# Kernel optimization log

Measured on AMD Instinct MI355X. Metric: run time of the kernel, lower is better.

## Reference

```python
import jax, jax.numpy as jnp
import numpy as np

# batches, users-per-batch (max_user_num), servers-per-batch (max_server_num), dims
B, U, S, DU, DS, H = 64, 256, 64, 16, 16, 256
DEG_S, DEG_U = 8, 16
NU, NS = B * U, B * S
IN_DIM = U * DU + S * DS  # 5120


def setup_inputs() -> dict:
    key = jax.random.key(0)
    ks = jax.random.split(key, 12)
    x_user = jax.random.normal(ks[0], (NU, DU), jnp.float32)
    x_server = jax.random.normal(ks[1], (NS, DS), jnp.float32)
    # within-batch edges: user u in batch u//U connects to servers/users of same batch
    src_u2s = jnp.repeat(jnp.arange(NU), DEG_S)
    dst_u2s = (src_u2s // U) * S + jax.random.randint(ks[2], (NU * DEG_S,), 0, S)
    src_u2u = jnp.repeat(jnp.arange(NU), DEG_U)
    dst_u2u = (src_u2u // U) * U + jax.random.randint(ks[3], (NU * DEG_U,), 0, U)

    def lin(k, i, o):
        return jax.random.normal(k, (i, o), jnp.float32) * 0.02

    params = dict(
        oW1=lin(ks[4], IN_DIM, H), ob1=jnp.zeros((H,), jnp.float32),
        oW2=lin(ks[5], H, H), ob2=jnp.zeros((H,), jnp.float32),
        oW3=lin(ks[6], H, 2), ob3=jnp.zeros((2,), jnp.float32),
        sW1=lin(ks[7], IN_DIM, H), sb1=jnp.zeros((H,), jnp.float32),
        sW2=lin(ks[8], H, H), sb2=jnp.zeros((H,), jnp.float32),
        sW3=lin(ks[9], H, S), sb3=jnp.zeros((S,), jnp.float32),
    )
    return dict(x_user=x_user, x_server=x_server,
                src_u2s=src_u2s, dst_u2s=dst_u2s,
                src_u2u=src_u2u, dst_u2u=dst_u2u, **params)


def _mlp3(x, W1, b1, W2, b2, W3, b3):
    h = jax.nn.relu(x @ W1 + b1)
    h = jax.nn.sigmoid(h @ W2 + b2)
    return h @ W3 + b3


def reference(x_user, x_server, src_u2s, dst_u2s, src_u2u, dst_u2u,
              oW1, ob1, oW2, ob2, oW3, ob3, sW1, sb1, sW2, sb2, sW3, sb3):
    # scatter neighbor features into per-user dense observation slots
    # (edges are within-batch, so dst % S / dst % U is the local slot index,
    #  identical to the original global-offset scatter + batch mask)
    server_obs = (jnp.zeros((NU, S, DS), x_server.dtype)
                  .at[src_u2s, dst_u2s % S].set(x_server[dst_u2s]))
    user_obs = (jnp.zeros((NU, U, DU), x_user.dtype)
                .at[src_u2u, dst_u2u % U].set(x_user[dst_u2u]))
    feats = jnp.concatenate([server_obs.reshape(B, U, S * DS),
                             user_obs.reshape(B, U, U * DU)], axis=-1)  # [B,U,IN_DIM]
    offloading_probs = jax.nn.softmax(
        _mlp3(feats, oW1, ob1, oW2, ob2, oW3, ob3), axis=-1)  # [B,U,2]
    sel_logits = _mlp3(feats, sW1, sb1, sW2, sb2, sW3, sb3)   # [B,U,S]
    # -inf mask: 0 only at (user, server) pairs connected by a u2s edge
    non_probs = (jnp.full((NU, S), -jnp.inf, jnp.float32)
                 .at[src_u2s, dst_u2s % S].set(0.0)
                 .reshape(B, U, S))
    selection_probs = jax.nn.softmax(sel_logits + non_probs, axis=-1)
    return offloading_probs, selection_probs
```

## Files before the change

kernel.cpp:

```cpp
#include <hip/hip_runtime.h>
#include <hip/hip_bf16.h>
#include <math.h>
#include <cstdint>

#define NUSER 16384
#define BB    64
#define UU    256
#define SSLOT 64
#define HD    256
#define KTOT  320
#define DEGS  8
#define DEGU  16

typedef __attribute__((ext_vector_type(8))) short short8;
typedef __attribute__((ext_vector_type(4))) float f32x4;

static __device__ __forceinline__ __hip_bfloat16 f2b(float x) { return __float2bfloat16(x); }
static __device__ __forceinline__ unsigned pack2(float x, float y) {
  union { __hip_bfloat16 h[2]; unsigned u; } cv;
  cv.h[0] = f2b(x); cv.h[1] = f2b(y);
  return cv.u;
}

__global__ __launch_bounds__(256) void k_prep_pq(
    const int* __restrict__ dst_u2s, const int* __restrict__ dst_u2u,
    const float* __restrict__ oW2, const float* __restrict__ sW2,
    const float* __restrict__ sW3,
    const float* __restrict__ xu, const float* __restrict__ xs,
    const float* __restrict__ oW1, const float* __restrict__ sW1,
    unsigned long long* __restrict__ connS, unsigned* __restrict__ MSUW,
    __hip_bfloat16* __restrict__ W2T_o, __hip_bfloat16* __restrict__ W2T_s,
    __hip_bfloat16* __restrict__ W3T_s,
    __hip_bfloat16* __restrict__ P_o, __hip_bfloat16* __restrict__ P_s,
    __hip_bfloat16* __restrict__ Q_o, __hip_bfloat16* __restrict__ Q_s) {
  const int t = threadIdx.x;
  if (blockIdx.y == 0) {
    const int blk = blockIdx.x;
    if (blk < 64) {
      const int u = blk * 256 + t;
      unsigned long long ms = 0ull;
      #pragma unroll
      for (int i = 0; i < DEGS; ++i) ms |= 1ull << (dst_u2s[u * DEGS + i] & 63);
      connS[u] = ms;
      unsigned long long m0 = 0, m1 = 0, m2 = 0, m3 = 0;
      #pragma unroll
      for (int i = 0; i < DEGU; ++i) {
        int slot = dst_u2u[u * DEGU + i] & 255;
        unsigned long long bit = 1ull << (slot & 63);
        int w = slot >> 6;
        if (w == 0) m0 |= bit; else if (w == 1) m1 |= bit;
        else if (w == 2) m2 |= bit; else m3 |= bit;
      }
      unsigned* mw = MSUW + (size_t)u * 10;
      uint2* mw2 = (uint2*)mw;
      mw2[0] = make_uint2((unsigned)ms, (unsigned)(ms >> 32));
      mw2[1] = make_uint2((unsigned)m0, (unsigned)(m0 >> 32));
      mw2[2] = make_uint2((unsigned)m1, (unsigned)(m1 >> 32));
      mw2[3] = make_uint2((unsigned)m2, (unsigned)(m2 >> 32));
      mw2[4] = make_uint2((unsigned)m3, (unsigned)(m3 >> 32));
    } else {
      const int n = blk - 64;
      W2T_o[n * HD + t] = f2b(oW2[t * HD + n]);
      W2T_s[n * HD + t] = f2b(sW2[t * HD + n]);
      if (n < SSLOT) W3T_s[n * HD + t] = f2b(sW3[t * SSLOT + n]);
    }
    return;
  }
  const int wg = blockIdx.x;
  const int b0 = (blockIdx.y - 1) * 8;
  __shared__ float lx[8 * 16];
  const bool isS = wg < SSLOT;
  const int slot = isS ? wg : wg - SSLOT;
  if (t < 8 * 16) {
    int b = b0 + (t >> 4), d = t & 15;
    lx[t] = isS ? xs[(b * SSLOT + slot) * 16 + d] : xu[(b * UU + slot) * 16 + d];
  }
  __syncthreads();
  float wo[16], wsv[16];
  const int rbase = isS ? slot * 16 : SSLOT * 16 + slot * 16;
  #pragma unroll
  for (int d = 0; d < 16; ++d) {
    wo[d] = oW1[(rbase + d) * HD + t];
    wsv[d] = sW1[(rbase + d) * HD + t];
  }
  __hip_bfloat16* Ro = isS ? P_o : Q_o;
  __hip_bfloat16* Rs = isS ? P_s : Q_s;
  const int rows = isS ? SSLOT : UU;
  #pragma unroll
  for (int bi = 0; bi < 8; ++bi) {
    float ao = 0.f, as = 0.f;
    #pragma unroll
    for (int q = 0; q < 4; ++q) {
      float4 x4 = *(const float4*)&lx[bi * 16 + q * 4];
      ao = fmaf(x4.x, wo[q*4+0], ao); as = fmaf(x4.x, wsv[q*4+0], as);
      ao = fmaf(x4.y, wo[q*4+1], ao); as = fmaf(x4.y, wsv[q*4+1], as);
      ao = fmaf(x4.z, wo[q*4+2], ao); as = fmaf(x4.z, wsv[q*4+2], as);
      ao = fmaf(x4.w, wo[q*4+3], ao); as = fmaf(x4.w, wsv[q*4+3], as);
    }
    Ro[((b0 + bi) * rows + slot) * HD + t] = f2b(ao);
    Rs[((b0 + bi) * rows + slot) * HD + t] = f2b(as);
  }
}

__global__ __launch_bounds__(256) void k_tr(
    const __hip_bfloat16* __restrict__ P_o, const __hip_bfloat16* __restrict__ P_s,
    const __hip_bfloat16* __restrict__ Q_o, const __hip_bfloat16* __restrict__ Q_s,
    __hip_bfloat16* __restrict__ PQT_o, __hip_bfloat16* __restrict__ PQT_s) {
  const int b = blockIdx.x, mlp = blockIdx.y, nc = blockIdx.z;
  const int n0 = nc * 64;
  const int t = threadIdx.x;
  const __hip_bfloat16* P = mlp ? P_s : P_o;
  const __hip_bfloat16* Q = mlp ? Q_s : Q_o;
  __hip_bfloat16* PQT = mlp ? PQT_s : PQT_o;
  __shared__ __align__(16) short lds[64 * 72];
  for (int kt = 0; kt < 5; ++kt) {
    const __hip_bfloat16* src = (kt == 0) ? (P + (size_t)(b * SSLOT) * HD)
                                          : (Q + (size_t)(b * UU + (kt - 1) * 64) * HD);
    const int kout = (kt == 0) ? 0 : 64 + (kt - 1) * 64;
    #pragma unroll
    for (int i = 0; i < 2; ++i) {
      int c = t + i * 256;
      int row = c >> 3, cc = c & 7;
      *(short8*)&lds[row * 72 + cc * 8] =
          *(const short8*)(src + (size_t)row * HD + n0 + cc * 8);
    }
    __syncthreads();
    #pragma unroll
    for (int i = 0; i < 2; ++i) {
      int c = t + i * 256;
      int nrow = c >> 3, kc = c & 7;
      short8 v;
      #pragma unroll
      for (int e = 0; e < 8; ++e) v[e] = lds[(kc * 8 + e) * 72 + nrow];
      *(short8*)(PQT + (size_t)(b * 256 + n0 + nrow) * KTOT + kout + kc * 8) = v;
    }
    __syncthreads();
  }
}

__global__ __launch_bounds__(512) void k_h1(
    const unsigned* __restrict__ MSUW,
    const __hip_bfloat16* __restrict__ PQT_o, const __hip_bfloat16* __restrict__ PQT_s,
    const float* __restrict__ ob1, const float* __restrict__ sb1,
    __hip_bfloat16* __restrict__ h1o, __hip_bfloat16* __restrict__ h1s) {
  const int b = blockIdx.x, mlp = blockIdx.y, nh = blockIdx.z;
  const int n0 = nh * 128;
  const int t = threadIdx.x;
  const __hip_bfloat16* PQT = mlp ? PQT_s : PQT_o;
  const float* b1 = mlp ? sb1 : ob1;
  __hip_bfloat16* h1 = mlp ? h1s : h1o;

  __shared__ __align__(16) short pan[128 * KTOT];
  __shared__ __align__(16) unsigned mskL[256 * 10];

  {
    const int r = t >> 2;
    const int c4 = t & 3;
    const __hip_bfloat16* src = PQT + (size_t)(b * 256 + n0 + r) * KTOT;
    #pragma unroll
    for (int i = 0; i < 10; ++i) {
      int cc = c4 + 4 * i;
      *(short8*)&pan[r * KTOT + ((cc ^ (r & 7)) * 8)] = *(const short8*)(src + cc * 8);
    }
  }
  {
    const uint2* g = (const uint2*)(MSUW + (size_t)b * 2560);
    uint2* l = (uint2*)mskL;
    l[t] = g[t];
    l[t + 512] = g[t + 512];
    if (t < 256) l[t + 1024] = g[t + 1024];
  }
  __syncthreads();

  const int lane = t & 63, w = t >> 6;
  const int wr = w >> 1, wc = w & 1;
  const int lo = lane & 15, hi = lane >> 4;
  f32x4 acc[4][4] = {};
  #pragma unroll
  for (int kt = 0; kt < 10; ++kt) {
    short8 af[4], bf[4];
    #pragma unroll
    for (int rb = 0; rb < 4; ++rb) {
      int ul = wr * 64 + rb * 16 + lo;
      unsigned m = mskL[ul * 10 + kt];
      unsigned by = (m >> (hi * 8)) & 0xFFu;
      union { unsigned u[4]; short8 s; } cv;
      cv.u[0] = ((by & 1u)   ? 0x3F80u : 0u) | ((by & 2u)   ? 0x3F800000u : 0u);
      cv.u[1] = ((by & 4u)   ? 0x3F80u : 0u) | ((by & 8u)   ? 0x3F800000u : 0u);
      cv.u[2] = ((by & 16u)  ? 0x3F80u : 0u) | ((by & 32u)  ? 0x3F800000u : 0u);
      cv.u[3] = ((by & 64u)  ? 0x3F80u : 0u) | ((by & 128u) ? 0x3F800000u : 0u);
      af[rb] = cv.s;
    }
    #pragma unroll
    for (int cb = 0; cb < 4; ++cb) {
      int n = wc * 64 + cb * 16 + lo;
      int cc = kt * 4 + hi;
      bf[cb] = *(const short8*)&pan[n * KTOT + ((cc ^ (n & 7)) * 8)];
    }
    #pragma unroll
    for (int rb = 0; rb < 4; ++rb)
      #pragma unroll
      for (int cb = 0; cb < 4; ++cb)
        acc[rb][cb] = __builtin_amdgcn_mfma_f32_16x16x32_bf16(af[rb], bf[cb], acc[rb][cb], 0, 0, 0);
  }
  #pragma unroll
  for (int cb = 0; cb < 4; ++cb) {
    int n = wc * 64 + cb * 16 + lo;
    float bv = b1[n0 + n];
    #pragma unroll
    for (int rb = 0; rb < 4; ++rb) {
      #pragma unroll
      for (int j = 0; j < 4; ++j) {
        int u = b * 256 + wr * 64 + rb * 16 + hi * 4 + j;
        h1[(size_t)u * HD + n0 + n] = f2b(fmaxf(acc[rb][cb][j] + bv, 0.f));
      }
    }
  }
}

__global__ __launch_bounds__(256) void k_heads(
    const __hip_bfloat16* __restrict__ h1o, const __hip_bfloat16* __restrict__ h1s,
    const __hip_bfloat16* __restrict__ W2T_o, const __hip_bfloat16* __restrict__ W2T_s,
    const float* __restrict__ ob2, const float* __restrict__ sb2,
    const float* __restrict__ oW3, const float* __restrict__ ob3,
    const __hip_bfloat16* __restrict__ W3T_s, const float* __restrict__ sb3,
    const unsigned long long* __restrict__ connS,
    float* __restrict__ out) {
  const int mlp = blockIdx.y;
  const int x = blockIdx.x;
  const int blk = (x & 7) * 64 + (x >> 3);
  const int u0 = blk * 32;
  const int t = threadIdx.x, lane = t & 63, wid = t >> 6;
  const int lo = lane & 15, hi = lane >> 4;

  const __hip_bfloat16* A   = mlp ? h1s : h1o;
  const __hip_bfloat16* W2T = mlp ? W2T_s : W2T_o;
  const float* b2 = mlp ? sb2 : ob2;

  __shared__ __align__(16) char lds[16384 + 36864];
  short* As = (short*)lds;
  short* Bs = (short*)(lds + 16384);
  float* part = (float*)lds;

  #pragma unroll
  for (int i = 0; i < 4; ++i) {
    int c = t + i * 256;
    int row = c >> 5, cc = c & 31;
    *(short8*)&As[row * 256 + (cc ^ (row & 7)) * 8] =
        *(const short8*)(A + (size_t)(u0 + row) * HD + cc * 8);
  }
  __syncthreads();

  f32x4 acc2[2][4] = {};
  for (int ks = 0; ks < 8; ++ks) {
    if (ks) __syncthreads();
    #pragma unroll
    for (int i = 0; i < 4; ++i) {
      int c = t + i * 256;
      int n = c >> 2, kc = c & 3;
      *(short8*)&Bs[n * 72 + kc * 8] =
          *(const short8*)(W2T + (size_t)n * HD + ks * 32 + kc * 8);
    }
    __syncthreads();
    short8 af[2], bf[4];
    #pragma unroll
    for (int rb = 0; rb < 2; ++rb) {
      int row = rb * 16 + lo;
      int ca = ks * 4 + hi;
      af[rb] = *(const short8*)&As[row * 256 + (ca ^ (row & 7)) * 8];
    }
    #pragma unroll
    for (int cb = 0; cb < 4; ++cb) {
      int n = wid * 64 + cb * 16 + lo;
      bf[cb] = *(const short8*)&Bs[n * 72 + hi * 8];
    }
    #pragma unroll
    for (int rb = 0; rb < 2; ++rb)
      #pragma unroll
      for (int cb = 0; cb < 4; ++cb)
        acc2[rb][cb] = __builtin_amdgcn_mfma_f32_16x16x32_bf16(af[rb], bf[cb], acc2[rb][cb], 0, 0, 0);
  }
  __syncthreads();

  if (mlp == 0) {
    float p0[2][4] = {}, p1[2][4] = {};
    #pragma unroll
    for (int cb = 0; cb < 4; ++cb) {
      int n = wid * 64 + cb * 16 + lo;
      float bs = b2[n], w0 = oW3[2 * n], w1 = oW3[2 * n + 1];
      #pragma unroll
      for (int rb = 0; rb < 2; ++rb)
        #pragma unroll
        for (int j = 0; j < 4; ++j) {
          float sig = 1.0f / (1.0f + __expf(-(acc2[rb][cb][j] + bs)));
          p0[rb][j] = fmaf(sig, w0, p0[rb][j]);
          p1[rb][j] = fmaf(sig, w1, p1[rb][j]);
        }
    }
    #pragma unroll
    for (int rb = 0; rb < 2; ++rb)
      #pragma unroll
      for (int j = 0; j < 4; ++j) {
        #pragma unroll
        for (int off = 1; off < 16; off <<= 1) {
          p0[rb][j] += __shfl_xor(p0[rb][j], off, 64);
          p1[rb][j] += __shfl_xor(p1[rb][j], off, 64);
        }
        if (lo == 0) {
          int row = rb * 16 + hi * 4 + j;
          part[wid * 64 + row * 2 + 0] = p0[rb][j];
          part[wid * 64 + row * 2 + 1] = p1[rb][j];
        }
      }
    __syncthreads();
    if (t < 32) {
      float q0 = part[t * 2] + part[64 + t * 2] + part[128 + t * 2] + part[192 + t * 2] + ob3[0];
      float q1 = part[t * 2 + 1] + part[64 + t * 2 + 1] + part[128 + t * 2 + 1] + part[192 + t * 2 + 1] + ob3[1];
      float m2 = fmaxf(q0, q1);
      float e0 = __expf(q0 - m2), e1 = __expf(q1 - m2);
      float iv = 1.0f / (e0 + e1);
      float2 r; r.x = e0 * iv; r.y = e1 * iv;
      *(float2*)(out + (size_t)(u0 + t) * 2) = r;
    }
  } else {
    short* sel = As;
    #pragma unroll
    for (int cb = 0; cb < 4; ++cb) {
      int n = wid * 64 + cb * 16 + lo;
      float bs = b2[n];
      #pragma unroll
      for (int rb = 0; rb < 2; ++rb)
        #pragma unroll
        for (int j = 0; j < 4; ++j) {
          int row = rb * 16 + hi * 4 + j;
          float sig = 1.0f / (1.0f + __expf(-(acc2[rb][cb][j] + bs)));
          sel[row * 256 + ((n >> 3) ^ (row & 7)) * 8 + (n & 7)] = (short)pack2(sig, 0.f);
        }
    }
    __syncthreads();
    if (wid < 2) {
      f32x4 acc3[4] = {};
      #pragma unroll
      for (int ks = 0; ks < 8; ++ks) {
        int row = wid * 16 + lo;
        int ca = ks * 4 + hi;
        short8 af = *(const short8*)&sel[row * 256 + (ca ^ (row & 7)) * 8];
        #pragma unroll
        for (int cb = 0; cb < 4; ++cb) {
          short8 bf = *(const short8*)(W3T_s + (size_t)(cb * 16 + lo) * HD + ks * 32 + hi * 8);
          acc3[cb] = __builtin_amdgcn_mfma_f32_16x16x32_bf16(af, bf, acc3[cb], 0, 0, 0);
        }
      }
      float sb3n[4];
      #pragma unroll
      for (int cb = 0; cb < 4; ++cb) sb3n[cb] = sb3[cb * 16 + lo];
      const int ubase = u0 + wid * 16 + hi * 4;
      #pragma unroll
      for (int j = 0; j < 4; ++j) {
        unsigned long long m = connS[ubase + j];
        float v[4]; bool ok[4];
        float mx = -INFINITY;
        #pragma unroll
        for (int cb = 0; cb < 4; ++cb) {
          int n = cb * 16 + lo;
          ok[cb] = (m >> n) & 1ull;
          v[cb] = ok[cb] ? (acc3[cb][j] + sb3n[cb]) : -INFINITY;
          mx = fmaxf(mx, v[cb]);
        }
        #pragma unroll
        for (int off = 1; off < 16; off <<= 1) mx = fmaxf(mx, __shfl_xor(mx, off, 64));
        float e[4], ssum = 0.f;
        #pragma unroll
        for (int cb = 0; cb < 4; ++cb) {
          e[cb] = ok[cb] ? __expf(v[cb] - mx) : 0.f;
          ssum += e[cb];
        }
        #pragma unroll
        for (int off = 1; off < 16; off <<= 1) ssum += __shfl_xor(ssum, off, 64);
        float iv = 1.0f / ssum;
        #pragma unroll
        for (int cb = 0; cb < 4; ++cb) {
          int n = cb * 16 + lo;
          out[(size_t)NUSER * 2 + (size_t)(ubase + j) * SSLOT + n] = e[cb] * iv;
        }
      }
    }
  }
}

extern "C" void kernel_launch(void* const* d_in, const int* in_sizes, int n_in,
                              void* d_out, int out_size, void* d_ws, size_t ws_size,
                              hipStream_t stream) {
  const float* x_user   = (const float*)d_in[0];
  const float* x_server = (const float*)d_in[1];
  const int*   dst_u2s  = (const int*)d_in[3];
  const int*   dst_u2u  = (const int*)d_in[5];
  const float* oW1 = (const float*)d_in[6];
  const float* ob1 = (const float*)d_in[7];
  const float* oW2 = (const float*)d_in[8];
  const float* ob2 = (const float*)d_in[9];
  const float* oW3 = (const float*)d_in[10];
  const float* ob3 = (const float*)d_in[11];
  const float* sW1 = (const float*)d_in[12];
  const float* sb1 = (const float*)d_in[13];
  const float* sW2 = (const float*)d_in[14];
  const float* sb2 = (const float*)d_in[15];
  const float* sW3 = (const float*)d_in[16];
  const float* sb3 = (const float*)d_in[17];

  char* ws = (char*)d_ws;
  unsigned long long* connS = (unsigned long long*)(ws + 0);
  unsigned*       MSUW = (unsigned*)(ws + 131072);
  __hip_bfloat16* P_o  = (__hip_bfloat16*)(ws + 786432);
  __hip_bfloat16* P_s  = (__hip_bfloat16*)(ws + 2883584);
  __hip_bfloat16* Q_o  = (__hip_bfloat16*)(ws + 4980736);
  __hip_bfloat16* Q_s  = (__hip_bfloat16*)(ws + 13369344);
  __hip_bfloat16* PQT_o = (__hip_bfloat16*)(ws + 21757952);
  __hip_bfloat16* PQT_s = (__hip_bfloat16*)(ws + 32243712);
  __hip_bfloat16* h1o  = (__hip_bfloat16*)(ws + 42729472);
  __hip_bfloat16* h1s  = (__hip_bfloat16*)(ws + 51118080);
  __hip_bfloat16* W2T_o = (__hip_bfloat16*)(ws + 59506688);
  __hip_bfloat16* W2T_s = (__hip_bfloat16*)(ws + 59637760);
  __hip_bfloat16* W3T_s = (__hip_bfloat16*)(ws + 59768832);
  float* out = (float*)d_out;

  k_prep_pq<<<dim3(320, 9), 256, 0, stream>>>(
      dst_u2s, dst_u2u, oW2, sW2, sW3, x_user, x_server, oW1, sW1,
      connS, MSUW, W2T_o, W2T_s, W3T_s, P_o, P_s, Q_o, Q_s);
  k_tr<<<dim3(64, 2, 4), 256, 0, stream>>>(P_o, P_s, Q_o, Q_s, PQT_o, PQT_s);
  k_h1<<<dim3(64, 2, 2), 512, 0, stream>>>(MSUW, PQT_o, PQT_s, ob1, sb1, h1o, h1s);
  k_heads<<<dim3(512, 2), 256, 0, stream>>>(h1o, h1s, W2T_o, W2T_s, ob2, sb2,
                                            oW3, ob3, W3T_s, sb3, connS, out);
}
```

Measured before the change: 61.01 us.

## Write projected features directly in transposed layout and drop transpose kernel

The projection kernel now remaps threads so each thread computes one (slot, hidden) pair and writes the bf16 result straight into the K-major PQT buffers, which removes the separate k_tr transpose kernel, one launch, and one intermediate round trip through global memory. The prep grid was reshaped to 320 blocks (5 slot groups × 64 hidden groups), so the W2/W3 transposes are redistributed across those blocks. The k_h1 GEMM is retiled to 256-thread blocks covering 128 users, with the K panel staged in two halves to reduce LDS use and double the block count. The cost is uncoalesced 2-byte scattered stores in the projection and per-thread redundant reads of x.

```diff
diff --git a/kernel.cpp b/kernel.cpp
--- a/kernel.cpp
+++ b/kernel.cpp
@@ -22,7 +22,7 @@
   return cv.u;
 }
 
-__global__ __launch_bounds__(256) void k_prep_pq(
+__global__ __launch_bounds__(256) void k_p1(
     const int* __restrict__ dst_u2s, const int* __restrict__ dst_u2u,
     const float* __restrict__ oW2, const float* __restrict__ sW2,
     const float* __restrict__ sW3,
@@ -31,13 +31,12 @@
     unsigned long long* __restrict__ connS, unsigned* __restrict__ MSUW,
     __hip_bfloat16* __restrict__ W2T_o, __hip_bfloat16* __restrict__ W2T_s,
     __hip_bfloat16* __restrict__ W3T_s,
-    __hip_bfloat16* __restrict__ P_o, __hip_bfloat16* __restrict__ P_s,
-    __hip_bfloat16* __restrict__ Q_o, __hip_bfloat16* __restrict__ Q_s) {
+    __hip_bfloat16* __restrict__ PQT_o, __hip_bfloat16* __restrict__ PQT_s) {
   const int t = threadIdx.x;
+  const int x = blockIdx.x;
   if (blockIdx.y == 0) {
-    const int blk = blockIdx.x;
-    if (blk < 64) {
-      const int u = blk * 256 + t;
+    if (x < 64) {
+      const int u = x * 256 + t;
       unsigned long long ms = 0ull;
       #pragma unroll
       for (int i = 0; i < DEGS; ++i) ms |= 1ull << (dst_u2s[u * DEGS + i] & 63);
@@ -51,167 +50,140 @@
         if (w == 0) m0 |= bit; else if (w == 1) m1 |= bit;
         else if (w == 2) m2 |= bit; else m3 |= bit;
       }
-      unsigned* mw = MSUW + (size_t)u * 10;
-      uint2* mw2 = (uint2*)mw;
+      uint2* mw2 = (uint2*)(MSUW + (size_t)u * 10);
       mw2[0] = make_uint2((unsigned)ms, (unsigned)(ms >> 32));
       mw2[1] = make_uint2((unsigned)m0, (unsigned)(m0 >> 32));
       mw2[2] = make_uint2((unsigned)m1, (unsigned)(m1 >> 32));
       mw2[3] = make_uint2((unsigned)m2, (unsigned)(m2 >> 32));
       mw2[4] = make_uint2((unsigned)m3, (unsigned)(m3 >> 32));
+      W3T_s[x * HD + t] = f2b(sW3[t * SSLOT + x]);
     } else {
-      const int n = blk - 64;
+      const int n = x - 64;
       W2T_o[n * HD + t] = f2b(oW2[t * HD + n]);
       W2T_s[n * HD + t] = f2b(sW2[t * HD + n]);
-      if (n < SSLOT) W3T_s[n * HD + t] = f2b(sW3[t * SSLOT + n]);
+      if (n < SSLOT) {
+        W2T_o[(n + 192) * HD + t] = f2b(oW2[t * HD + n + 192]);
+        W2T_s[(n + 192) * HD + t] = f2b(sW2[t * HD + n + 192]);
+      }
     }
     return;
   }
-  const int wg = blockIdx.x;
   const int b0 = (blockIdx.y - 1) * 8;
-  __shared__ float lx[8 * 16];
-  const bool isS = wg < SSLOT;
-  const int slot = isS ? wg : wg - SSLOT;
-  if (t < 8 * 16) {
-    int b = b0 + (t >> 4), d = t & 15;
-    lx[t] = isS ? xs[(b * SSLOT + slot) * 16 + d] : xu[(b * UU + slot) * 16 + d];
-  }
-  __syncthreads();
+  const int sg = x >> 6, ng = x & 63;
+  const int s = t & 63, ni = t >> 6;
+  const int n = ng * 4 + ni;
+  const int rbase = (sg == 0) ? s * 16 : 1024 + ((sg - 1) * 64 + s) * 16;
   float wo[16], wsv[16];
-  const int rbase = isS ? slot * 16 : SSLOT * 16 + slot * 16;
   #pragma unroll
   for (int d = 0; d < 16; ++d) {
-    wo[d] = oW1[(rbase + d) * HD + t];
-    wsv[d] = sW1[(rbase + d) * HD + t];
-  }
-  __hip_bfloat16* Ro = isS ? P_o : Q_o;
-  __hip_bfloat16* Rs = isS ? P_s : Q_s;
-  const int rows = isS ? SSLOT : UU;
+    wo[d]  = oW1[(rbase + d) * HD + n];
+    wsv[d] = sW1[(rbase + d) * HD + n];
+  }
+  const float* xbase = (sg == 0) ? xs : (xu + (size_t)(sg - 1) * 64 * 16);
+  const int xstride = (sg == 0) ? 1024 : 4096;
+  const int kk = sg * 64 + s;
   #pragma unroll
   for (int bi = 0; bi < 8; ++bi) {
-    float ao = 0.f, as = 0.f;
-    #pragma unroll
-    for (int q = 0; q < 4; ++q) {
-      float4 x4 = *(const float4*)&lx[bi * 16 + q * 4];
-      ao = fmaf(x4.x, wo[q*4+0], ao); as = fmaf(x4.x, wsv[q*4+0], as);
-      ao = fmaf(x4.y, wo[q*4+1], ao); as = fmaf(x4.y, wsv[q*4+1], as);
-      ao = fmaf(x4.z, wo[q*4+2], ao); as = fmaf(x4.z, wsv[q*4+2], as);
-      ao = fmaf(x4.w, wo[q*4+3], ao); as = fmaf(x4.w, wsv[q*4+3], as);
-    }
-    Ro[((b0 + bi) * rows + slot) * HD + t] = f2b(ao);
-    Rs[((b0 + bi) * rows + slot) * HD + t] = f2b(as);
+    const int b = b0 + bi;
+    const float4* xp = (const float4*)(xbase + (size_t)b * xstride + s * 16);
+    float4 x0 = xp[0], x1 = xp[1], x2 = xp[2], x3 = xp[3];
+    float ao, as;
+    ao  = x0.x * wo[0];  as  = x0.x * wsv[0];
+    ao = fmaf(x0.y, wo[1], ao);  as = fmaf(x0.y, wsv[1], as);
+    ao = fmaf(x0.z, wo[2], ao);  as = fmaf(x0.z, wsv[2], as);
+    ao = fmaf(x0.w, wo[3], ao);  as = fmaf(x0.w, wsv[3], as);
+    ao = fmaf(x1.x, wo[4], ao);  as = fmaf(x1.x, wsv[4], as);
+    ao = fmaf(x1.y, wo[5], ao);  as = fmaf(x1.y, wsv[5], as);
+    ao = fmaf(x1.z, wo[6], ao);  as = fmaf(x1.z, wsv[6], as);
+    ao = fmaf(x1.w, wo[7], ao);  as = fmaf(x1.w, wsv[7], as);
+    ao = fmaf(x2.x, wo[8], ao);  as = fmaf(x2.x, wsv[8], as);
+    ao = fmaf(x2.y, wo[9], ao);  as = fmaf(x2.y, wsv[9], as);
+    ao = fmaf(x2.z, wo[10], ao); as = fmaf(x2.z, wsv[10], as);
+    ao = fmaf(x2.w, wo[11], ao); as = fmaf(x2.w, wsv[11], as);
+    ao = fmaf(x3.x, wo[12], ao); as = fmaf(x3.x, wsv[12], as);
+    ao = fmaf(x3.y, wo[13], ao); as = fmaf(x3.y, wsv[13], as);
+    ao = fmaf(x3.z, wo[14], ao); as = fmaf(x3.z, wsv[14], as);
+    ao = fmaf(x3.w, wo[15], ao); as = fmaf(x3.w, wsv[15], as);
+    const size_t off = (size_t)(b * 256 + n) * KTOT + kk;
+    PQT_o[off] = f2b(ao);
+    PQT_s[off] = f2b(as);
   }
 }
 
-__global__ __launch_bounds__(256) void k_tr(
-    const __hip_bfloat16* __restrict__ P_o, const __hip_bfloat16* __restrict__ P_s,
-    const __hip_bfloat16* __restrict__ Q_o, const __hip_bfloat16* __restrict__ Q_s,
-    __hip_bfloat16* __restrict__ PQT_o, __hip_bfloat16* __restrict__ PQT_s) {
-  const int b = blockIdx.x, mlp = blockIdx.y, nc = blockIdx.z;
-  const int n0 = nc * 64;
-  const int t = threadIdx.x;
-  const __hip_bfloat16* P = mlp ? P_s : P_o;
-  const __hip_bfloat16* Q = mlp ? Q_s : Q_o;
-  __hip_bfloat16* PQT = mlp ? PQT_s : PQT_o;
-  __shared__ __align__(16) short lds[64 * 72];
-  for (int kt = 0; kt < 5; ++kt) {
-    const __hip_bfloat16* src = (kt == 0) ? (P + (size_t)(b * SSLOT) * HD)
-                                          : (Q + (size_t)(b * UU + (kt - 1) * 64) * HD);
-    const int kout = (kt == 0) ? 0 : 64 + (kt - 1) * 64;
-    #pragma unroll
-    for (int i = 0; i < 2; ++i) {
-      int c = t + i * 256;
-      int row = c >> 3, cc = c & 7;
-      *(short8*)&lds[row * 72 + cc * 8] =
-          *(const short8*)(src + (size_t)row * HD + n0 + cc * 8);
-    }
-    __syncthreads();
-    #pragma unroll
-    for (int i = 0; i < 2; ++i) {
-      int c = t + i * 256;
-      int nrow = c >> 3, kc = c & 7;
-      short8 v;
-      #pragma unroll
-      for (int e = 0; e < 8; ++e) v[e] = lds[(kc * 8 + e) * 72 + nrow];
-      *(short8*)(PQT + (size_t)(b * 256 + n0 + nrow) * KTOT + kout + kc * 8) = v;
-    }
-    __syncthreads();
-  }
-}
-
-__global__ __launch_bounds__(512) void k_h1(
+__global__ __launch_bounds__(256) void k_h1(
     const unsigned* __restrict__ MSUW,
     const __hip_bfloat16* __restrict__ PQT_o, const __hip_bfloat16* __restrict__ PQT_s,
     const float* __restrict__ ob1, const float* __restrict__ sb1,
     __hip_bfloat16* __restrict__ h1o, __hip_bfloat16* __restrict__ h1s) {
-  const int b = blockIdx.x, mlp = blockIdx.y, nh = blockIdx.z;
+  const int b = blockIdx.x >> 1, uh = blockIdx.x & 1;
+  const int mlp = blockIdx.y, nh = blockIdx.z;
   const int n0 = nh * 128;
   const int t = threadIdx.x;
   const __hip_bfloat16* PQT = mlp ? PQT_s : PQT_o;
   const float* b1 = mlp ? sb1 : ob1;
   __hip_bfloat16* h1 = mlp ? h1s : h1o;
 
-  __shared__ __align__(16) short pan[128 * KTOT];
-  __shared__ __align__(16) unsigned mskL[256 * 10];
+  __shared__ __align__(16) char smem[48128];
+  short* pan = (short*)smem;
+  unsigned* mskL = (unsigned*)(smem + 43008);
 
   {
-    const int r = t >> 2;
-    const int c4 = t & 3;
-    const __hip_bfloat16* src = PQT + (size_t)(b * 256 + n0 + r) * KTOT;
-    #pragma unroll
-    for (int i = 0; i < 10; ++i) {
-      int cc = c4 + 4 * i;
-      *(short8*)&pan[r * KTOT + ((cc ^ (r & 7)) * 8)] = *(const short8*)(src + cc * 8);
-    }
-  }
-  {
-    const uint2* g = (const uint2*)(MSUW + (size_t)b * 2560);
-    uint2* l = (uint2*)mskL;
-    l[t] = g[t];
-    l[t + 512] = g[t + 512];
-    if (t < 256) l[t + 1024] = g[t + 1024];
-  }
-  __syncthreads();
-
+    const unsigned* g = MSUW + (size_t)(b * 256 + uh * 128) * 10;
+    #pragma unroll
+    for (int i = 0; i < 5; ++i) mskL[t + 256 * i] = g[t + 256 * i];
+  }
   const int lane = t & 63, w = t >> 6;
-  const int wr = w >> 1, wc = w & 1;
   const int lo = lane & 15, hi = lane >> 4;
-  f32x4 acc[4][4] = {};
+  f32x4 acc[2][8] = {};
+  for (int kc = 0; kc < 2; ++kc) {
+    if (kc) __syncthreads();
+    {
+      const int r = t >> 1, c4 = t & 1;
+      const __hip_bfloat16* src = PQT + (size_t)(b * 256 + n0 + r) * KTOT + kc * 160;
+      #pragma unroll
+      for (int i = 0; i < 10; ++i) {
+        int cc = c4 + 2 * i;
+        *(short8*)&pan[r * 168 + cc * 8] = *(const short8*)(src + cc * 8);
+      }
+    }
+    __syncthreads();
+    #pragma unroll
+    for (int kt2 = 0; kt2 < 5; ++kt2) {
+      const int kt = kc * 5 + kt2;
+      short8 af[2], bf[8];
+      #pragma unroll
+      for (int rb = 0; rb < 2; ++rb) {
+        int lu = w * 32 + rb * 16 + lo;
+        unsigned m = mskL[lu * 10 + kt];
+        unsigned by = (m >> (hi * 8)) & 0xFFu;
+        union { unsigned u[4]; short8 s; } cv;
+        cv.u[0] = ((by & 1u)  ? 0x3F80u : 0u) | ((by & 2u)   ? 0x3F800000u : 0u);
+        cv.u[1] = ((by & 4u)  ? 0x3F80u : 0u) | ((by & 8u)   ? 0x3F800000u : 0u);
+        cv.u[2] = ((by & 16u) ? 0x3F80u : 0u) | ((by & 32u)  ? 0x3F800000u : 0u);
+        cv.u[3] = ((by & 64u) ? 0x3F80u : 0u) | ((by & 128u) ? 0x3F800000u : 0u);
+        af[rb] = cv.s;
+      }
+      #pragma unroll
+      for (int cb = 0; cb < 8; ++cb) {
+        int n = cb * 16 + lo;
+        bf[cb] = *(const short8*)&pan[n * 168 + (kt2 * 4 + hi) * 8];
+      }
+      #pragma unroll
+      for (int rb = 0; rb < 2; ++rb)
+        #pragma unroll
+        for (int cb = 0; cb < 8; ++cb)
+          acc[rb][cb] = __builtin_amdgcn_mfma_f32_16x16x32_bf16(af[rb], bf[cb], acc[rb][cb], 0, 0, 0);
+    }
+  }
   #pragma unroll
-  for (int kt = 0; kt < 10; ++kt) {
-    short8 af[4], bf[4];
-    #pragma unroll
-    for (int rb = 0; rb < 4; ++rb) {
-      int ul = wr * 64 + rb * 16 + lo;
-      unsigned m = mskL[ul * 10 + kt];
-      unsigned by = (m >> (hi * 8)) & 0xFFu;
-      union { unsigned u[4]; short8 s; } cv;
-      cv.u[0] = ((by & 1u)   ? 0x3F80u : 0u) | ((by & 2u)   ? 0x3F800000u : 0u);
-      cv.u[1] = ((by & 4u)   ? 0x3F80u : 0u) | ((by & 8u)   ? 0x3F800000u : 0u);
-      cv.u[2] = ((by & 16u)  ? 0x3F80u : 0u) | ((by & 32u)  ? 0x3F800000u : 0u);
-      cv.u[3] = ((by & 64u)  ? 0x3F80u : 0u) | ((by & 128u) ? 0x3F800000u : 0u);
-      af[rb] = cv.s;
-    }
-    #pragma unroll
-    for (int cb = 0; cb < 4; ++cb) {
-      int n = wc * 64 + cb * 16 + lo;
-      int cc = kt * 4 + hi;
-      bf[cb] = *(const short8*)&pan[n * KTOT + ((cc ^ (n & 7)) * 8)];
-    }
-    #pragma unroll
-    for (int rb = 0; rb < 4; ++rb)
-      #pragma unroll
-      for (int cb = 0; cb < 4; ++cb)
-        acc[rb][cb] = __builtin_amdgcn_mfma_f32_16x16x32_bf16(af[rb], bf[cb], acc[rb][cb], 0, 0, 0);
-  }
-  #pragma unroll
-  for (int cb = 0; cb < 4; ++cb) {
-    int n = wc * 64 + cb * 16 + lo;
+  for (int cb = 0; cb < 8; ++cb) {
+    int n = cb * 16 + lo;
     float bv = b1[n0 + n];
     #pragma unroll
-    for (int rb = 0; rb < 4; ++rb) {
+    for (int rb = 0; rb < 2; ++rb) {
       #pragma unroll
       for (int j = 0; j < 4; ++j) {
-        int u = b * 256 + wr * 64 + rb * 16 + hi * 4 + j;
+        int u = b * 256 + uh * 128 + w * 32 + rb * 16 + hi * 4 + j;
         h1[(size_t)u * HD + n0 + n] = f2b(fmaxf(acc[rb][cb][j] + bv, 0.f));
       }
     }
@@ -410,25 +382,20 @@
 
   char* ws = (char*)d_ws;
   unsigned long long* connS = (unsigned long long*)(ws + 0);
-  unsigned*       MSUW = (unsigned*)(ws + 131072);
-  __hip_bfloat16* P_o  = (__hip_bfloat16*)(ws + 786432);
-  __hip_bfloat16* P_s  = (__hip_bfloat16*)(ws + 2883584);
-  __hip_bfloat16* Q_o  = (__hip_bfloat16*)(ws + 4980736);
-  __hip_bfloat16* Q_s  = (__hip_bfloat16*)(ws + 13369344);
-  __hip_bfloat16* PQT_o = (__hip_bfloat16*)(ws + 21757952);
-  __hip_bfloat16* PQT_s = (__hip_bfloat16*)(ws + 32243712);
-  __hip_bfloat16* h1o  = (__hip_bfloat16*)(ws + 42729472);
-  __hip_bfloat16* h1s  = (__hip_bfloat16*)(ws + 51118080);
-  __hip_bfloat16* W2T_o = (__hip_bfloat16*)(ws + 59506688);
-  __hip_bfloat16* W2T_s = (__hip_bfloat16*)(ws + 59637760);
-  __hip_bfloat16* W3T_s = (__hip_bfloat16*)(ws + 59768832);
+  unsigned*       MSUW  = (unsigned*)(ws + 131072);
+  __hip_bfloat16* PQT_o = (__hip_bfloat16*)(ws + 786432);
+  __hip_bfloat16* PQT_s = (__hip_bfloat16*)(ws + 11272192);
+  __hip_bfloat16* h1o   = (__hip_bfloat16*)(ws + 21757952);
+  __hip_bfloat16* h1s   = (__hip_bfloat16*)(ws + 30146560);
+  __hip_bfloat16* W2T_o = (__hip_bfloat16*)(ws + 38535168);
+  __hip_bfloat16* W2T_s = (__hip_bfloat16*)(ws + 38666240);
+  __hip_bfloat16* W3T_s = (__hip_bfloat16*)(ws + 38797312);
   float* out = (float*)d_out;
 
-  k_prep_pq<<<dim3(320, 9), 256, 0, stream>>>(
+  k_p1<<<dim3(320, 9), 256, 0, stream>>>(
       dst_u2s, dst_u2u, oW2, sW2, sW3, x_user, x_server, oW1, sW1,
-      connS, MSUW, W2T_o, W2T_s, W3T_s, P_o, P_s, Q_o, Q_s);
-  k_tr<<<dim3(64, 2, 4), 256, 0, stream>>>(P_o, P_s, Q_o, Q_s, PQT_o, PQT_s);
-  k_h1<<<dim3(64, 2, 2), 512, 0, stream>>>(MSUW, PQT_o, PQT_s, ob1, sb1, h1o, h1s);
+      connS, MSUW, W2T_o, W2T_s, W3T_s, PQT_o, PQT_s);
+  k_h1<<<dim3(128, 2, 2), 256, 0, stream>>>(MSUW, PQT_o, PQT_s, ob1, sb1, h1o, h1s);
   k_heads<<<dim3(512, 2), 256, 0, stream>>>(h1o, h1s, W2T_o, W2T_s, ob2, sb2,
                                             oW3, ob3, W3T_s, sb3, connS, out);
 }
```

After: 161.6 us. +164.8%, slower.

## Split k_h1 across user halves and stage K panel in two chunks

Applied to the files above, without the earlier changes.

k_h1 now launches twice as many blocks, each with 256 threads covering 128 users instead of 256. The B panel is staged in LDS in two K-halves of 160 with padded rows (stride 168) instead of the full 320-wide XOR-swizzled panel. This cuts LDS per block from about 92KB to 48KB so more blocks fit per CU and the grid fills the GPU better. The cost is an extra barrier between chunks, each PQT panel being read twice (once per user half), and each wave computing a 32x128 tile that needs more accumulator registers.

```diff
diff --git a/kernel.cpp b/kernel.cpp
--- a/kernel.cpp
+++ b/kernel.cpp
@@ -138,80 +138,80 @@
   }
 }
 
-__global__ __launch_bounds__(512) void k_h1(
+__global__ __launch_bounds__(256) void k_h1(
     const unsigned* __restrict__ MSUW,
     const __hip_bfloat16* __restrict__ PQT_o, const __hip_bfloat16* __restrict__ PQT_s,
     const float* __restrict__ ob1, const float* __restrict__ sb1,
     __hip_bfloat16* __restrict__ h1o, __hip_bfloat16* __restrict__ h1s) {
-  const int b = blockIdx.x, mlp = blockIdx.y, nh = blockIdx.z;
+  const int b = blockIdx.x >> 1, uh = blockIdx.x & 1;
+  const int mlp = blockIdx.y, nh = blockIdx.z;
   const int n0 = nh * 128;
   const int t = threadIdx.x;
   const __hip_bfloat16* PQT = mlp ? PQT_s : PQT_o;
   const float* b1 = mlp ? sb1 : ob1;
   __hip_bfloat16* h1 = mlp ? h1s : h1o;
 
-  __shared__ __align__(16) short pan[128 * KTOT];
-  __shared__ __align__(16) unsigned mskL[256 * 10];
+  __shared__ __align__(16) char smem[48128];
+  short* pan = (short*)smem;
+  unsigned* mskL = (unsigned*)(smem + 43008);
 
   {
-    const int r = t >> 2;
-    const int c4 = t & 3;
-    const __hip_bfloat16* src = PQT + (size_t)(b * 256 + n0 + r) * KTOT;
-    #pragma unroll
-    for (int i = 0; i < 10; ++i) {
-      int cc = c4 + 4 * i;
-      *(short8*)&pan[r * KTOT + ((cc ^ (r & 7)) * 8)] = *(const short8*)(src + cc * 8);
-    }
-  }
-  {
-    const uint2* g = (const uint2*)(MSUW + (size_t)b * 2560);
-    uint2* l = (uint2*)mskL;
-    l[t] = g[t];
-    l[t + 512] = g[t + 512];
-    if (t < 256) l[t + 1024] = g[t + 1024];
-  }
-  __syncthreads();
-
+    const unsigned* g = MSUW + (size_t)(b * 256 + uh * 128) * 10;
+    #pragma unroll
+    for (int i = 0; i < 5; ++i) mskL[t + 256 * i] = g[t + 256 * i];
+  }
   const int lane = t & 63, w = t >> 6;
-  const int wr = w >> 1, wc = w & 1;
   const int lo = lane & 15, hi = lane >> 4;
-  f32x4 acc[4][4] = {};
+  f32x4 acc[2][8] = {};
+  for (int kc = 0; kc < 2; ++kc) {
+    if (kc) __syncthreads();
+    {
+      const int r = t >> 1, c4 = t & 1;
+      const __hip_bfloat16* src = PQT + (size_t)(b * 256 + n0 + r) * KTOT + kc * 160;
+      #pragma unroll
+      for (int i = 0; i < 10; ++i) {
+        int cc = c4 + 2 * i;
+        *(short8*)&pan[r * 168 + cc * 8] = *(const short8*)(src + cc * 8);
+      }
+    }
+    __syncthreads();
+    #pragma unroll
+    for (int kt2 = 0; kt2 < 5; ++kt2) {
+      const int kt = kc * 5 + kt2;
+      short8 af[2], bf[8];
+      #pragma unroll
+      for (int rb = 0; rb < 2; ++rb) {
+        int lu = w * 32 + rb * 16 + lo;
+        unsigned m = mskL[lu * 10 + kt];
+        unsigned by = (m >> (hi * 8)) & 0xFFu;
+        union { unsigned u[4]; short8 s; } cv;
+        cv.u[0] = ((by & 1u)  ? 0x3F80u : 0u) | ((by & 2u)   ? 0x3F800000u : 0u);
+        cv.u[1] = ((by & 4u)  ? 0x3F80u : 0u) | ((by & 8u)   ? 0x3F800000u : 0u);
+        cv.u[2] = ((by & 16u) ? 0x3F80u : 0u) | ((by & 32u)  ? 0x3F800000u : 0u);
+        cv.u[3] = ((by & 64u) ? 0x3F80u : 0u) | ((by & 128u) ? 0x3F800000u : 0u);
+        af[rb] = cv.s;
+      }
+      #pragma unroll
+      for (int cb = 0; cb < 8; ++cb) {
+        int n = cb * 16 + lo;
+        bf[cb] = *(const short8*)&pan[n * 168 + (kt2 * 4 + hi) * 8];
+      }
+      #pragma unroll
+      for (int rb = 0; rb < 2; ++rb)
+        #pragma unroll
+        for (int cb = 0; cb < 8; ++cb)
+          acc[rb][cb] = __builtin_amdgcn_mfma_f32_16x16x32_bf16(af[rb], bf[cb], acc[rb][cb], 0, 0, 0);
+    }
+  }
   #pragma unroll
-  for (int kt = 0; kt < 10; ++kt) {
-    short8 af[4], bf[4];
-    #pragma unroll
-    for (int rb = 0; rb < 4; ++rb) {
-      int ul = wr * 64 + rb * 16 + lo;
-      unsigned m = mskL[ul * 10 + kt];
-      unsigned by = (m >> (hi * 8)) & 0xFFu;
-      union { unsigned u[4]; short8 s; } cv;
-      cv.u[0] = ((by & 1u)   ? 0x3F80u : 0u) | ((by & 2u)   ? 0x3F800000u : 0u);
-      cv.u[1] = ((by & 4u)   ? 0x3F80u : 0u) | ((by & 8u)   ? 0x3F800000u : 0u);
-      cv.u[2] = ((by & 16u)  ? 0x3F80u : 0u) | ((by & 32u)  ? 0x3F800000u : 0u);
-      cv.u[3] = ((by & 64u)  ? 0x3F80u : 0u) | ((by & 128u) ? 0x3F800000u : 0u);
-      af[rb] = cv.s;
-    }
-    #pragma unroll
-    for (int cb = 0; cb < 4; ++cb) {
-      int n = wc * 64 + cb * 16 + lo;
-      int cc = kt * 4 + hi;
-      bf[cb] = *(const short8*)&pan[n * KTOT + ((cc ^ (n & 7)) * 8)];
-    }
-    #pragma unroll
-    for (int rb = 0; rb < 4; ++rb)
-      #pragma unroll
-      for (int cb = 0; cb < 4; ++cb)
-        acc[rb][cb] = __builtin_amdgcn_mfma_f32_16x16x32_bf16(af[rb], bf[cb], acc[rb][cb], 0, 0, 0);
-  }
-  #pragma unroll
-  for (int cb = 0; cb < 4; ++cb) {
-    int n = wc * 64 + cb * 16 + lo;
+  for (int cb = 0; cb < 8; ++cb) {
+    int n = cb * 16 + lo;
     float bv = b1[n0 + n];
     #pragma unroll
-    for (int rb = 0; rb < 4; ++rb) {
+    for (int rb = 0; rb < 2; ++rb) {
       #pragma unroll
       for (int j = 0; j < 4; ++j) {
-        int u = b * 256 + wr * 64 + rb * 16 + hi * 4 + j;
+        int u = b * 256 + uh * 128 + w * 32 + rb * 16 + hi * 4 + j;
         h1[(size_t)u * HD + n0 + n] = f2b(fmaxf(acc[rb][cb][j] + bv, 0.f));
       }
     }
@@ -410,7 +410,7 @@
 
   char* ws = (char*)d_ws;
   unsigned long long* connS = (unsigned long long*)(ws + 0);
-  unsigned*       MSUW = (unsigned*)(ws + 131072);
+  unsigned*       MSUW  = (unsigned*)(ws + 131072);
   __hip_bfloat16* P_o  = (__hip_bfloat16*)(ws + 786432);
   __hip_bfloat16* P_s  = (__hip_bfloat16*)(ws + 2883584);
   __hip_bfloat16* Q_o  = (__hip_bfloat16*)(ws + 4980736);
@@ -428,7 +428,7 @@
       dst_u2s, dst_u2u, oW2, sW2, sW3, x_user, x_server, oW1, sW1,
       connS, MSUW, W2T_o, W2T_s, W3T_s, P_o, P_s, Q_o, Q_s);
   k_tr<<<dim3(64, 2, 4), 256, 0, stream>>>(P_o, P_s, Q_o, Q_s, PQT_o, PQT_s);
-  k_h1<<<dim3(64, 2, 2), 512, 0, stream>>>(MSUW, PQT_o, PQT_s, ob1, sb1, h1o, h1s);
+  k_h1<<<dim3(128, 2, 2), 256, 0, stream>>>(MSUW, PQT_o, PQT_s, ob1, sb1, h1o, h1s);
   k_heads<<<dim3(512, 2), 256, 0, stream>>>(h1o, h1s, W2T_o, W2T_s, ob2, sb2,
                                             oW3, ob3, W3T_s, sb3, connS, out);
 }
```

Result: no change. 60.29 us (-1.2%).
